# Kernel tuning notes

Hardware: AMD Instinct MI355X
Metric: run time of the kernel (lower is better)

The kernel has to match this reference:

```python
import jax, jax.numpy as jnp
import numpy as np

B, S, E, H = 4, 2048, 1024, 16
DH = E // H


def setup_inputs() -> dict:
    key = jax.random.key(0)
    ks = jax.random.split(key, 8)
    sc = 0.02
    inp = {
        "v": jax.random.normal(ks[0], (B, S, E), jnp.float32),
        "k": jax.random.normal(ks[1], (B, S, E), jnp.float32),
        "q": jax.random.normal(ks[2], (B, S, E), jnp.float32),
        # causal mask, broadcast over batch and heads; 0 => masked
        "mask": jnp.tril(jnp.ones((S, S), jnp.int32))[None, None, :, :],
        "wq": jax.random.normal(ks[3], (E, E), jnp.float32) * sc,
        "bq": jnp.zeros((E,), jnp.float32),
        "wk": jax.random.normal(ks[4], (E, E), jnp.float32) * sc,
        "bk": jnp.zeros((E,), jnp.float32),
        "wv": jax.random.normal(ks[5], (E, E), jnp.float32) * sc,
        "bv": jnp.zeros((E,), jnp.float32),
        "wo": jax.random.normal(ks[6], (E, E), jnp.float32) * sc,
        "bo": jnp.zeros((E,), jnp.float32),
    }
    return inp


def _split_heads(x):
    # [B,S,E] -> [B,H,S,DH]
    b, s, _ = x.shape
    return x.reshape(b, s, H, DH).transpose(0, 2, 1, 3)


def reference(v, k, q, mask, wq, bq, wk, bk, wv, bv, wo, bo):
    # Linear layers (torch Linear: x @ W^T + b)
    qh = _split_heads(q @ wq.T + bq)
    kh = _split_heads(k @ wk.T + bk)
    vh = _split_heads(v @ wv.T + bv)
    scale = 1.0 / jnp.sqrt(jnp.asarray(DH, qh.dtype))
    scores = jnp.einsum("bhqd,bhkd->bhqk", qh, kh) * scale  # [B,H,S,S]
    scores = jnp.where(mask == 0, -jnp.inf, scores)
    attn = jax.nn.softmax(scores, axis=-1)
    # dropout p=0.0 -> identity
    x = jnp.einsum("bhqk,bhkd->bhqd", attn, vh)  # [B,H,S,DH]
    x = x.transpose(0, 2, 1, 3).reshape(x.shape[0], -1, E)  # [B,S,E]
    return x @ wo.T + bo
```

## Files before the change

### kernel.cpp

```cpp
#include <hip/hip_runtime.h>
#include <hip/hip_bf16.h>

#define B_  4
#define S_  2048
#define E_  1024
#define H_  16
#define DH_ 64
constexpr int M_ = B_ * S_;
constexpr int K_ = E_;
constexpr int N_ = E_;
constexpr long NE_ = (long)B_ * S_ * E_;
constexpr long EE_ = (long)E_ * E_;

typedef __attribute__((ext_vector_type(8))) short bf16x8;
typedef __attribute__((ext_vector_type(4))) short bf16x4;
typedef __attribute__((ext_vector_type(4))) float f32x4;

__device__ __forceinline__ unsigned short f2bf(float f) {
    union { float f; unsigned u; } a; a.f = f;
    unsigned u = a.u;
    return (unsigned short)((u + 0x7fffu + ((u >> 16) & 1u)) >> 16);
}
__device__ __forceinline__ unsigned short f2bf_fast(float f) {
    union { float f; unsigned u; } a; a.f = f;
    return (unsigned short)((a.u + 0x8000u) >> 16);
}

__device__ __forceinline__ void async_copy16(const unsigned short* g, unsigned short* l) {
    __builtin_amdgcn_global_load_lds(
        (const __attribute__((address_space(1))) void*)g,
        (__attribute__((address_space(3))) void*)l, 16, 0, 0);
}

__device__ __forceinline__ f32x4 mfma16(bf16x4 a, bf16x4 b, f32x4 c) {
    return __builtin_amdgcn_mfma_f32_16x16x16bf16_1k(a, b, c, 0, 0, 0);
}

__global__ void cast3(const float* __restrict__ i0, const float* __restrict__ i1,
                      const float* __restrict__ i2,
                      unsigned short* __restrict__ o0, unsigned short* __restrict__ o1,
                      unsigned short* __restrict__ o2, int n4) {
    const float* in = blockIdx.y == 0 ? i0 : (blockIdx.y == 1 ? i1 : i2);
    unsigned short* out = blockIdx.y == 0 ? o0 : (blockIdx.y == 1 ? o1 : o2);
    int i = blockIdx.x * blockDim.x + threadIdx.x;
    if (i >= n4) return;
    float4 v = ((const float4*)in)[i];
    ushort4 o;
    o.x = f2bf(v.x); o.y = f2bf(v.y); o.z = f2bf(v.z); o.w = f2bf(v.w);
    ((ushort4*)out)[i] = o;
}

__global__ void cast4(const float* __restrict__ i0, const float* __restrict__ i1,
                      const float* __restrict__ i2, const float* __restrict__ i3,
                      unsigned short* __restrict__ o0, unsigned short* __restrict__ o1,
                      unsigned short* __restrict__ o2, unsigned short* __restrict__ o3,
                      int n4) {
    int y = blockIdx.y;
    const float* in = y == 0 ? i0 : (y == 1 ? i1 : (y == 2 ? i2 : i3));
    unsigned short* out = y == 0 ? o0 : (y == 1 ? o1 : (y == 2 ? o2 : o3));
    int i = blockIdx.x * blockDim.x + threadIdx.x;
    if (i >= n4) return;
    float4 v = ((const float4*)in)[i];
    ushort4 o;
    o.x = f2bf(v.x); o.y = f2bf(v.y); o.z = f2bf(v.z); o.w = f2bf(v.w);
    ((ushort4*)out)[i] = o;
}

__device__ __forceinline__ void gemm_core(
    const unsigned short* __restrict__ A, const unsigned short* __restrict__ Bw,
    unsigned short* sA, unsigned short* sB, int bm, int bn,
    int wave, int lane, f32x4 (*acc)[4]) {
    const int lane15 = lane & 15;
    const int laneq  = lane >> 4;
    const int waveM = wave & 1, waveN = wave >> 1;
    const int lrow = lane >> 3;
    const int lcol = (lane & 7) * 8;

    for (int k0 = 0; k0 < K_; k0 += 64) {
        __syncthreads();
        for (int c = wave; c < 16; c += 4) {
            const unsigned short* gA = A + (long)(bm * 128 + c * 8 + lrow) * K_ + k0 + lcol;
            async_copy16(gA, &sA[c * 512]);
            const unsigned short* gB = Bw + (long)(bn * 128 + c * 8 + lrow) * K_ + k0 + lcol;
            async_copy16(gB, &sB[c * 512]);
        }
        __syncthreads();
#pragma unroll
        for (int ks = 0; ks < 2; ++ks) {
            const int kc = ks * 32 + laneq * 8;
            bf16x8 af[4], bfr[4];
#pragma unroll
            for (int mi = 0; mi < 4; ++mi)
                af[mi] = *(const bf16x8*)&sA[(waveM * 64 + mi * 16 + lane15) * 64 + kc];
#pragma unroll
            for (int ni = 0; ni < 4; ++ni)
                bfr[ni] = *(const bf16x8*)&sB[(waveN * 64 + ni * 16 + lane15) * 64 + kc];
#pragma unroll
            for (int mi = 0; mi < 4; ++mi)
#pragma unroll
                for (int ni = 0; ni < 4; ++ni)
                    acc[mi][ni] = __builtin_amdgcn_mfma_f32_16x16x32_bf16(
                        af[mi], bfr[ni], acc[mi][ni], 0, 0, 0);
        }
    }
}

__global__ __launch_bounds__(256, 2)
void gemm3(const unsigned short* __restrict__ A0, const unsigned short* __restrict__ A1,
           const unsigned short* __restrict__ A2,
           const unsigned short* __restrict__ W0, const unsigned short* __restrict__ W1,
           const unsigned short* __restrict__ W2,
           const float* __restrict__ b0, const float* __restrict__ b1,
           const float* __restrict__ b2,
           unsigned short* __restrict__ o0, unsigned short* __restrict__ o1,
           unsigned short* __restrict__ o2, float osc0) {
    __shared__ __align__(16) unsigned short sA[128 * 64];
    __shared__ __align__(16) unsigned short sB[128 * 64];
    const int z = blockIdx.z;
    const unsigned short* A  = z == 0 ? A0 : (z == 1 ? A1 : A2);
    const unsigned short* Bw = z == 0 ? W0 : (z == 1 ? W1 : W2);
    const float* bias        = z == 0 ? b0 : (z == 1 ? b1 : b2);
    unsigned short* Out      = z == 0 ? o0 : (z == 1 ? o1 : o2);
    const float oscale = z == 0 ? osc0 : 1.0f;

    const int tid = threadIdx.x, wave = tid >> 6, lane = tid & 63;
    const int lane15 = lane & 15, laneq = lane >> 4;
    const int bm = blockIdx.x, bn = blockIdx.y;
    const int waveM = wave & 1, waveN = wave >> 1;

    f32x4 acc[4][4] = {};
    gemm_core(A, Bw, sA, sB, bm, bn, wave, lane, acc);

#pragma unroll
    for (int mi = 0; mi < 4; ++mi) {
        const int mbase = bm * 128 + waveM * 64 + mi * 16 + laneq * 4;
#pragma unroll
        for (int ni = 0; ni < 4; ++ni) {
            const int n = bn * 128 + waveN * 64 + ni * 16 + lane15;
            const float bv = bias[n];
#pragma unroll
            for (int r = 0; r < 4; ++r) {
                const int m = mbase + r;
                const float v = (acc[mi][ni][r] + bv) * oscale;
                const int b = m >> 11, s = m & (S_ - 1);
                const int h = n >> 6, d = n & (DH_ - 1);
                long idx;
                if (z == 2) idx = ((long)(b * H_ + h) * DH_ + d) * S_ + s;
                else        idx = ((long)(b * H_ + h) * S_ + s) * DH_ + d;
                Out[idx] = f2bf(v);
            }
        }
    }
}

__global__ __launch_bounds__(256, 2)
void gemm_out(const unsigned short* __restrict__ A, const unsigned short* __restrict__ Bw,
              const float* __restrict__ bias, float* __restrict__ Out) {
    __shared__ __align__(16) unsigned short sA[128 * 64];
    __shared__ __align__(16) unsigned short sB[128 * 64];
    const int tid = threadIdx.x, wave = tid >> 6, lane = tid & 63;
    const int lane15 = lane & 15, laneq = lane >> 4;
    const int bm = blockIdx.x, bn = blockIdx.y;
    const int waveM = wave & 1, waveN = wave >> 1;

    f32x4 acc[4][4] = {};
    gemm_core(A, Bw, sA, sB, bm, bn, wave, lane, acc);

#pragma unroll
    for (int mi = 0; mi < 4; ++mi) {
        const int mbase = bm * 128 + waveM * 64 + mi * 16 + laneq * 4;
#pragma unroll
        for (int ni = 0; ni < 4; ++ni) {
            const int n = bn * 128 + waveN * 64 + ni * 16 + lane15;
            const float bv = bias[n];
#pragma unroll
            for (int r = 0; r < 4; ++r)
                Out[(long)(mbase + r) * N_ + n] = acc[mi][ni][r] + bv;
        }
    }
}

constexpr int ALDK = 72;

__global__ __launch_bounds__(256)
void attn_kernel(const unsigned short* __restrict__ qh,
                 const unsigned short* __restrict__ kh,
                 const unsigned short* __restrict__ vT,
                 unsigned short* __restrict__ ctx) {
    __shared__ __align__(16) unsigned short sK[64 * ALDK];
    __shared__ __align__(16) unsigned short sV[64 * ALDK];

    const int tid = threadIdx.x;
    const int wave = tid >> 6, lane = tid & 63;
    const int lane15 = lane & 15, quad = lane >> 4;
    const int qs = 15 - blockIdx.x;
    const int bh = blockIdx.y;
    const long headQ = (long)bh * S_ * DH_;
    const long headV = (long)bh * DH_ * S_;
    const int qbase = qs * 128 + wave * 32;

    bf16x4 qf[2][4];
#pragma unroll
    for (int f = 0; f < 2; ++f) {
        const unsigned short* qrow = qh + headQ + (long)(qbase + f * 16 + lane15) * DH_;
#pragma unroll
        for (int c = 0; c < 4; ++c)
            qf[f][c] = *(const bf16x4*)(qrow + c * 16 + quad * 4);
    }

    f32x4 oT[2][4] = {};
    float rs[2] = {0.f, 0.f};

    const int ktmax = 2 * qs + 2;
    for (int kt = 0; kt < ktmax; ++kt) {
        const int k0 = kt * 64;
        __syncthreads();
        for (int it = tid; it < 512; it += 256) {
            const int row = it >> 3, col = (it & 7) * 8;
            *(bf16x8*)&sK[row * ALDK + col] =
                *(const bf16x8*)(kh + headQ + (long)(k0 + row) * DH_ + col);
            *(bf16x8*)&sV[row * ALDK + col] =
                *(const bf16x8*)(vT + headV + (long)row * S_ + k0 + col);
        }
        __syncthreads();

        f32x4 st[2][4] = {};
#pragma unroll
        for (int t = 0; t < 4; ++t) {
#pragma unroll
            for (int c = 0; c < 4; ++c) {
                bf16x4 kf = *(const bf16x4*)&sK[(t * 16 + lane15) * ALDK + c * 16 + quad * 4];
                st[0][t] = mfma16(kf, qf[0][c], st[0][t]);
                st[1][t] = mfma16(kf, qf[1][c], st[1][t]);
            }
        }

        bf16x4 pf[2][4];
        const bool need_mask = (k0 + 63 > qbase);
        if (need_mask) {
#pragma unroll
            for (int f = 0; f < 2; ++f) {
                const int qg = qbase + f * 16 + lane15;
#pragma unroll
                for (int t = 0; t < 4; ++t) {
                    const int kg = k0 + t * 16 + quad * 4;
#pragma unroll
                    for (int r = 0; r < 4; ++r) {
                        float s = (kg + r > qg) ? -1e30f : st[f][t][r];
                        const float p = __builtin_amdgcn_exp2f(s);
                        rs[f] += p;
                        pf[f][t][r] = (short)f2bf_fast(p);
                    }
                }
            }
        } else {
#pragma unroll
            for (int f = 0; f < 2; ++f)
#pragma unroll
                for (int t = 0; t < 4; ++t)
#pragma unroll
                    for (int r = 0; r < 4; ++r) {
                        const float p = __builtin_amdgcn_exp2f(st[f][t][r]);
                        rs[f] += p;
                        pf[f][t][r] = (short)f2bf_fast(p);
                    }
        }

#pragma unroll
        for (int dt = 0; dt < 4; ++dt) {
#pragma unroll
            for (int t = 0; t < 4; ++t) {
                bf16x4 vf = *(const bf16x4*)&sV[(dt * 16 + lane15) * ALDK + t * 16 + quad * 4];
                oT[0][dt] = mfma16(vf, pf[0][t], oT[0][dt]);
                oT[1][dt] = mfma16(vf, pf[1][t], oT[1][dt]);
            }
        }
    }

    float rinv[2];
#pragma unroll
    for (int f = 0; f < 2; ++f) {
        float v = rs[f];
        v += __shfl_xor(v, 16);
        v += __shfl_xor(v, 32);
        rinv[f] = 1.0f / v;
    }

    const int b = bh >> 4, h = bh & 15;
#pragma unroll
    for (int f = 0; f < 2; ++f) {
        const int qg = qbase + f * 16 + lane15;
        unsigned short* crow = ctx + ((long)b * S_ + qg) * E_ + h * 64;
#pragma unroll
        for (int dt = 0; dt < 4; ++dt) {
            ushort4 o;
            o.x = f2bf(oT[f][dt][0] * rinv[f]);
            o.y = f2bf(oT[f][dt][1] * rinv[f]);
            o.z = f2bf(oT[f][dt][2] * rinv[f]);
            o.w = f2bf(oT[f][dt][3] * rinv[f]);
            *(ushort4*)(crow + dt * 16 + quad * 4) = o;
        }
    }
}

extern "C" void kernel_launch(void* const* d_in, const int* in_sizes, int n_in,
                              void* d_out, int out_size, void* d_ws, size_t ws_size,
                              hipStream_t stream) {
    const float* v_in = (const float*)d_in[0];
    const float* k_in = (const float*)d_in[1];
    const float* q_in = (const float*)d_in[2];
    const float* wq = (const float*)d_in[4];
    const float* bq = (const float*)d_in[5];
    const float* wk = (const float*)d_in[6];
    const float* bk = (const float*)d_in[7];
    const float* wv = (const float*)d_in[8];
    const float* bv = (const float*)d_in[9];
    const float* wo = (const float*)d_in[10];
    const float* bo = (const float*)d_in[11];

    unsigned short* qb   = (unsigned short*)d_ws;
    unsigned short* kb   = qb + NE_;
    unsigned short* vb   = kb + NE_;
    unsigned short* wqb  = vb + NE_;
    unsigned short* wkb  = wqb + EE_;
    unsigned short* wvb  = wkb + EE_;
    unsigned short* wob  = wvb + EE_;
    unsigned short* qhb  = wob + EE_;
    unsigned short* khb  = qhb + NE_;
    unsigned short* vTb  = khb + NE_;
    unsigned short* ctxb = qb;

    const int n4a = (int)(NE_ / 4);
    const int n4w = (int)(EE_ / 4);
    cast3<<<dim3(n4a / 256, 3), 256, 0, stream>>>(q_in, k_in, v_in, qb, kb, vb, n4a);
    cast4<<<dim3(n4w / 256, 4), 256, 0, stream>>>(wq, wk, wv, wo, wqb, wkb, wvb, wob, n4w);

    const float QSCALE = 0.125f * 1.44269504089f;

    gemm3<<<dim3(M_ / 128, N_ / 128, 3), 256, 0, stream>>>(
        qb, kb, vb, wqb, wkb, wvb, bq, bk, bv, qhb, khb, vTb, QSCALE);

    attn_kernel<<<dim3(16, B_ * H_), 256, 0, stream>>>(qhb, khb, vTb, ctxb);

    gemm_out<<<dim3(M_ / 128, N_ / 128), 256, 0, stream>>>(ctxb, wob, bo, (float*)d_out);
}
```

Before: 409.5 us.

## Switch attention to 32x32x16 MFMA with LDS-staged P and paired causal tiles

Rewrites the attention kernel to use 32x32x16 bf16 MFMA for both QK^T and PV, staging the softmax probabilities through a per-wave LDS buffer to re-layout them as the A operand. Each block now pairs a short query tile with its mirror long tile (x and 31-x) to balance causal work across blocks, and sets occupancy via launch bounds. This aims to raise MFMA throughput and even out block durations, at the cost of extra LDS traffic, scalar 2-byte stores for P, and more row-sum registers and shuffles.

After: 398.2 us. 1.03x faster.

```diff
diff --git a/kernel.cpp b/kernel.cpp
--- a/kernel.cpp
+++ b/kernel.cpp
@@ -13,8 +13,8 @@
 constexpr long EE_ = (long)E_ * E_;
 
 typedef __attribute__((ext_vector_type(8))) short bf16x8;
-typedef __attribute__((ext_vector_type(4))) short bf16x4;
 typedef __attribute__((ext_vector_type(4))) float f32x4;
+typedef __attribute__((ext_vector_type(16))) float f32x16;
 
 __device__ __forceinline__ unsigned short f2bf(float f) {
     union { float f; unsigned u; } a; a.f = f;
@@ -30,10 +30,6 @@
     __builtin_amdgcn_global_load_lds(
         (const __attribute__((address_space(1))) void*)g,
         (__attribute__((address_space(3))) void*)l, 16, 0, 0);
-}
-
-__device__ __forceinline__ f32x4 mfma16(bf16x4 a, bf16x4 b, f32x4 c) {
-    return __builtin_amdgcn_mfma_f32_16x16x16bf16_1k(a, b, c, 0, 0, 0);
 }
 
 __global__ void cast3(const float* __restrict__ i0, const float* __restrict__ i1,
@@ -182,37 +178,43 @@
 
 constexpr int ALDK = 72;
 
-__global__ __launch_bounds__(256)
+__global__ __launch_bounds__(256, 4)
 void attn_kernel(const unsigned short* __restrict__ qh,
                  const unsigned short* __restrict__ kh,
                  const unsigned short* __restrict__ vT,
                  unsigned short* __restrict__ ctx) {
     __shared__ __align__(16) unsigned short sK[64 * ALDK];
     __shared__ __align__(16) unsigned short sV[64 * ALDK];
+    __shared__ __align__(16) unsigned short sP[128 * ALDK];
 
     const int tid = threadIdx.x;
     const int wave = tid >> 6, lane = tid & 63;
-    const int lane15 = lane & 15, quad = lane >> 4;
-    const int qs = 15 - blockIdx.x;
+    const int l31 = lane & 31, lhi = lane >> 5;
+    const int x = blockIdx.x;
     const int bh = blockIdx.y;
+    const int qta = x, qtb = 31 - x;
+    const bool isB = wave >= 2;
+    const int qrow0 = (isB ? qtb : qta) * 64 + (wave & 1) * 32;
     const long headQ = (long)bh * S_ * DH_;
     const long headV = (long)bh * DH_ * S_;
-    const int qbase = qs * 128 + wave * 32;
-
-    bf16x4 qf[2][4];
-#pragma unroll
-    for (int f = 0; f < 2; ++f) {
-        const unsigned short* qrow = qh + headQ + (long)(qbase + f * 16 + lane15) * DH_;
-#pragma unroll
-        for (int c = 0; c < 4; ++c)
-            qf[f][c] = *(const bf16x4*)(qrow + c * 16 + quad * 4);
-    }
-
-    f32x4 oT[2][4] = {};
-    float rs[2] = {0.f, 0.f};
-
-    const int ktmax = 2 * qs + 2;
-    for (int kt = 0; kt < ktmax; ++kt) {
+
+    bf16x8 qf[4];
+    {
+        const unsigned short* qrow = qh + headQ + (long)(qrow0 + l31) * DH_ + lhi * 8;
+        qf[0] = *(const bf16x8*)(qrow);
+        qf[1] = *(const bf16x8*)(qrow + 16);
+        qf[2] = *(const bf16x8*)(qrow + 32);
+        qf[3] = *(const bf16x8*)(qrow + 48);
+    }
+
+    f32x16 oacc[2] = {};
+    float rs[16];
+#pragma unroll
+    for (int i = 0; i < 16; ++i) rs[i] = 0.f;
+
+    unsigned short* myP = sP + wave * 32 * ALDK;
+
+    for (int kt = 0; kt <= qtb; ++kt) {
         const int k0 = kt * 64;
         __syncthreads();
         for (int it = tid; it < 512; it += 256) {
@@ -224,82 +226,59 @@
         }
         __syncthreads();
 
-        f32x4 st[2][4] = {};
-#pragma unroll
-        for (int t = 0; t < 4; ++t) {
-#pragma unroll
-            for (int c = 0; c < 4; ++c) {
-                bf16x4 kf = *(const bf16x4*)&sK[(t * 16 + lane15) * ALDK + c * 16 + quad * 4];
-                st[0][t] = mfma16(kf, qf[0][c], st[0][t]);
-                st[1][t] = mfma16(kf, qf[1][c], st[1][t]);
+        if (!isB && kt > qta) continue;
+
+        f32x16 st[2] = {};
+#pragma unroll
+        for (int kg = 0; kg < 2; ++kg)
+#pragma unroll
+            for (int ch = 0; ch < 4; ++ch) {
+                bf16x8 kf = *(const bf16x8*)&sK[(kg * 32 + l31) * ALDK + ch * 16 + lhi * 8];
+                st[kg] = __builtin_amdgcn_mfma_f32_32x32x16_bf16(qf[ch], kf, st[kg], 0, 0, 0);
             }
-        }
-
-        bf16x4 pf[2][4];
-        const bool need_mask = (k0 + 63 > qbase);
-        if (need_mask) {
-#pragma unroll
-            for (int f = 0; f < 2; ++f) {
-                const int qg = qbase + f * 16 + lane15;
-#pragma unroll
-                for (int t = 0; t < 4; ++t) {
-                    const int kg = k0 + t * 16 + quad * 4;
-#pragma unroll
-                    for (int r = 0; r < 4; ++r) {
-                        float s = (kg + r > qg) ? -1e30f : st[f][t][r];
-                        const float p = __builtin_amdgcn_exp2f(s);
-                        rs[f] += p;
-                        pf[f][t][r] = (short)f2bf_fast(p);
-                    }
-                }
+
+        const bool needmask = (k0 + 63 > qrow0);
+#pragma unroll
+        for (int kg = 0; kg < 2; ++kg) {
+            const int colg = k0 + kg * 32 + l31;
+#pragma unroll
+            for (int i = 0; i < 16; ++i) {
+                const int rloc = (i & 3) + 8 * (i >> 2) + 4 * lhi;
+                float s = st[kg][i];
+                if (needmask && colg > qrow0 + rloc) s = -1e30f;
+                const float p = __builtin_amdgcn_exp2f(s);
+                rs[i] += p;
+                myP[rloc * ALDK + kg * 32 + l31] = f2bf_fast(p);
             }
-        } else {
-#pragma unroll
-            for (int f = 0; f < 2; ++f)
-#pragma unroll
-                for (int t = 0; t < 4; ++t)
-#pragma unroll
-                    for (int r = 0; r < 4; ++r) {
-                        const float p = __builtin_amdgcn_exp2f(st[f][t][r]);
-                        rs[f] += p;
-                        pf[f][t][r] = (short)f2bf_fast(p);
-                    }
-        }
-
-#pragma unroll
-        for (int dt = 0; dt < 4; ++dt) {
-#pragma unroll
-            for (int t = 0; t < 4; ++t) {
-                bf16x4 vf = *(const bf16x4*)&sV[(dt * 16 + lane15) * ALDK + t * 16 + quad * 4];
-                oT[0][dt] = mfma16(vf, pf[0][t], oT[0][dt]);
-                oT[1][dt] = mfma16(vf, pf[1][t], oT[1][dt]);
+        }
+
+#pragma unroll
+        for (int kc = 0; kc < 4; ++kc) {
+            bf16x8 pf = *(const bf16x8*)&myP[l31 * ALDK + kc * 16 + lhi * 8];
+#pragma unroll
+            for (int dg = 0; dg < 2; ++dg) {
+                bf16x8 vf = *(const bf16x8*)&sV[(dg * 32 + l31) * ALDK + kc * 16 + lhi * 8];
+                oacc[dg] = __builtin_amdgcn_mfma_f32_32x32x16_bf16(pf, vf, oacc[dg], 0, 0, 0);
             }
         }
     }
 
-    float rinv[2];
-#pragma unroll
-    for (int f = 0; f < 2; ++f) {
-        float v = rs[f];
-        v += __shfl_xor(v, 16);
-        v += __shfl_xor(v, 32);
-        rinv[f] = 1.0f / v;
+    float rinv[16];
+#pragma unroll
+    for (int i = 0; i < 16; ++i) {
+        float v = rs[i];
+        v += __shfl_xor(v, 1); v += __shfl_xor(v, 2); v += __shfl_xor(v, 4);
+        v += __shfl_xor(v, 8); v += __shfl_xor(v, 16);
+        rinv[i] = 1.0f / v;
     }
 
     const int b = bh >> 4, h = bh & 15;
 #pragma unroll
-    for (int f = 0; f < 2; ++f) {
-        const int qg = qbase + f * 16 + lane15;
-        unsigned short* crow = ctx + ((long)b * S_ + qg) * E_ + h * 64;
-#pragma unroll
-        for (int dt = 0; dt < 4; ++dt) {
-            ushort4 o;
-            o.x = f2bf(oT[f][dt][0] * rinv[f]);
-            o.y = f2bf(oT[f][dt][1] * rinv[f]);
-            o.z = f2bf(oT[f][dt][2] * rinv[f]);
-            o.w = f2bf(oT[f][dt][3] * rinv[f]);
-            *(ushort4*)(crow + dt * 16 + quad * 4) = o;
-        }
+    for (int i = 0; i < 16; ++i) {
+        const int rloc = (i & 3) + 8 * (i >> 2) + 4 * lhi;
+        unsigned short* crow = ctx + ((long)b * S_ + qrow0 + rloc) * E_ + h * 64 + l31;
+        crow[0]  = f2bf(oacc[0][i] * rinv[i]);
+        crow[32] = f2bf(oacc[1][i] * rinv[i]);
     }
 }
 
```
